# Kernel tuning notes

Measured on AMD Instinct MI355X. Metric: run time of the kernel, lower is better.

Reference implementation:

```python
import jax, jax.numpy as jnp
import numpy as np

N, E, F_IN, F_OUT, PERIODS = 40000, 640000, 64, 128, 12


def setup_inputs() -> dict:
    key = jax.random.key(0)
    ks = jax.random.split(key, 24)
    def w(k, shape):
        return jax.random.normal(k, shape, jnp.float32) * 0.05
    inp = {
        "X": jax.random.normal(ks[0], (N, F_IN, PERIODS), jnp.float32),
        "edge_index": jax.random.randint(ks[1], (2, E), 0, N),
        "edge_weight": jax.random.uniform(ks[2], (E,), jnp.float32),
        "attention": jax.random.uniform(ks[3], (PERIODS,), jnp.float32),
    }
    for idx, g in enumerate(["i", "f", "c", "o"]):
        inp[f"W_x{g}"] = w(ks[4 + 4 * idx], (F_IN, F_OUT))
        inp[f"b_x{g}"] = jnp.zeros((F_OUT,), jnp.float32)
        inp[f"W_h{g}"] = w(ks[5 + 4 * idx], (2 * F_OUT, F_OUT))
        inp[f"b_h{g}"] = jnp.zeros((F_OUT,), jnp.float32)
    return inp


def reference(X, edge_index, edge_weight, attention,
              W_xi, b_xi, W_hi, b_hi,
              W_xf, b_xf, W_hf, b_hf,
              W_xc, b_xc, W_hc, b_hc,
              W_xo, b_xo, W_ho, b_ho):
    n = X.shape[0]
    # GCN normalization with self-loops: D^-1/2 (A + I) D^-1/2
    loops = jnp.arange(n)
    rows = jnp.concatenate([edge_index[0], loops])  # sources
    cols = jnp.concatenate([edge_index[1], loops])  # targets
    wts = jnp.concatenate([edge_weight, jnp.ones((n,), X.dtype)])
    deg = jax.ops.segment_sum(wts, cols, num_segments=n)
    dinv = jnp.where(deg > 0, jax.lax.rsqrt(deg), 0.0)
    norm = dinv[rows] * wts * dinv[cols]  # [E+N]

    def gcn(x, W, b):
        xw = x @ W  # [N, F_OUT]
        agg = jax.ops.segment_sum(norm[:, None] * xw[rows], cols, num_segments=n)
        return agg + b

    probs = jax.nn.softmax(attention)
    H0 = jnp.zeros((n, W_hi.shape[1]), X.dtype)
    C0 = jnp.zeros_like(H0)
    Xp = jnp.moveaxis(X, 2, 0)  # [periods, N, F_IN]

    def step(carry, xs):
        H, C, Hacc = carry
        x_t, p = xs
        def gate(Wx, bx, Wh, bh):
            return jnp.concatenate([gcn(x_t, Wx, bx), H], axis=1) @ Wh + bh
        I = jax.nn.sigmoid(gate(W_xi, b_xi, W_hi, b_hi))
        F = jax.nn.sigmoid(gate(W_xf, b_xf, W_hf, b_hf))
        Ct = jnp.tanh(gate(W_xc, b_xc, W_hc, b_hc))
        O = jax.nn.sigmoid(gate(W_xo, b_xo, W_ho, b_ho))
        C_new = F * C + I * Ct
        H_new = O * jnp.tanh(C_new)
        return (H_new, C_new, Hacc + p * H_new), None

    (H, C, Hacc), _ = jax.lax.scan(step, (H0, C0, H0), (Xp, probs))
    return Hacc
```

## Files before the change

### kernel.cpp

```cpp
#include <hip/hip_runtime.h>

typedef __bf16 bf16_t;
typedef bf16_t bf16x4 __attribute__((ext_vector_type(4)));
typedef bf16_t bf16x8 __attribute__((ext_vector_type(8)));
typedef float floatx4 __attribute__((ext_vector_type(4)));

#define F_INq 64
#define F_OUTq 128
#define PERIODSq 12
#define XROW (F_INq * PERIODSq)

__global__ __launch_bounds__(256) void k_init(float* deg, int* counts, int N) {
  int i = blockIdx.x * 256 + threadIdx.x;
  if (i < N) { deg[i] = 1.0f; counts[i] = 0; }
}

__global__ __launch_bounds__(256) void k_accum(const int* __restrict__ ei, const float* __restrict__ ew,
                                               float* deg, int* counts, int E) {
  int e = blockIdx.x * 256 + threadIdx.x;
  if (e < E) {
    int c = ei[E + e];
    atomicAdd(&deg[c], ew[e]);
    atomicAdd(&counts[c], 1);
  }
}

__global__ __launch_bounds__(256) void k_dinv(float* deg, int N) {
  int i = blockIdx.x * 256 + threadIdx.x;
  if (i < N) { float d = deg[i]; deg[i] = d > 0.0f ? rsqrtf(d) : 0.0f; }
}

__global__ __launch_bounds__(1024) void k_scan(const int* __restrict__ counts, int* __restrict__ offs,
                                               int* __restrict__ cursor, int N) {
  __shared__ int sd[1024];
  int t = threadIdx.x;
  int CH = (N + 1023) >> 10;
  int base = t * CH;
  int sum = 0;
  for (int i = 0; i < CH; ++i) { int idx = base + i; if (idx < N) sum += counts[idx]; }
  sd[t] = sum;
  __syncthreads();
  for (int off = 1; off < 1024; off <<= 1) {
    int v = (t >= off) ? sd[t - off] : 0;
    __syncthreads();
    sd[t] += v;
    __syncthreads();
  }
  int run = sd[t] - sum;
  for (int i = 0; i < CH; ++i) {
    int idx = base + i;
    if (idx < N) { offs[idx] = run; cursor[idx] = run; run += counts[idx]; }
  }
  if (t == 1023) offs[N] = sd[1023];
}

__global__ __launch_bounds__(256) void k_scatter(const int* __restrict__ ei, const float* __restrict__ ew,
                                                 const float* __restrict__ dinv, int* cursor,
                                                 int* __restrict__ csr_src, float* __restrict__ csr_nrm, int E) {
  int e = blockIdx.x * 256 + threadIdx.x;
  if (e < E) {
    int r = ei[e], c = ei[E + e];
    int p = atomicAdd(&cursor[c], 1);
    csr_src[p] = r;
    csr_nrm[p] = dinv[r] * ew[e] * dinv[c];
  }
}

__global__ __launch_bounds__(256) void k_prew(
    const float* __restrict__ Wxi, const float* __restrict__ Whi,
    const float* __restrict__ Wxf, const float* __restrict__ Whf,
    const float* __restrict__ Wxc, const float* __restrict__ Whc,
    const float* __restrict__ Wxo, const float* __restrict__ Who,
    const float* __restrict__ bxi, const float* __restrict__ bhi,
    const float* __restrict__ bxf, const float* __restrict__ bhf,
    const float* __restrict__ bxc, const float* __restrict__ bhc,
    const float* __restrict__ bxo, const float* __restrict__ bho,
    const float* __restrict__ att,
    bf16_t* __restrict__ WbT, float* __restrict__ bcomb, float* __restrict__ probs) {
  const int WT = 512 * 192;
  int gid = blockIdx.x * 256 + threadIdx.x;
  if (gid < WT) {
    int col = gid / 192, k = gid % 192;
    int g = col >> 7, j = col & 127;
    const float* Wx = g == 0 ? Wxi : g == 1 ? Wxf : g == 2 ? Wxc : Wxo;
    const float* Wh = g == 0 ? Whi : g == 1 ? Whf : g == 2 ? Whc : Who;
    float s;
    if (k < 64) {
      s = 0.0f;
      for (int kk = 0; kk < 128; ++kk) s += Wx[k * 128 + kk] * Wh[kk * 128 + j];
    } else {
      s = Wh[(k + 64) * 128 + j];
    }
    WbT[(size_t)col * 192 + k] = (bf16_t)s;
  } else if (gid < WT + 512) {
    int cc = gid - WT;
    int g = cc >> 7, j = cc & 127;
    const float* bx = g == 0 ? bxi : g == 1 ? bxf : g == 2 ? bxc : bxo;
    const float* bh = g == 0 ? bhi : g == 1 ? bhf : g == 2 ? bhc : bho;
    const float* Wh = g == 0 ? Whi : g == 1 ? Whf : g == 2 ? Whc : Who;
    float s = bh[j];
    for (int kk = 0; kk < 128; ++kk) s += bx[kk] * Wh[kk * 128 + j];
    bcomb[cc] = s;
  } else if (gid == WT + 512) {
    float m = att[0];
    for (int i = 1; i < PERIODSq; ++i) m = fmaxf(m, att[i]);
    float e[PERIODSq], s = 0.0f;
    for (int i = 0; i < PERIODSq; ++i) { e[i] = __expf(att[i] - m); s += e[i]; }
    for (int i = 0; i < PERIODSq; ++i) probs[i] = e[i] / s;
  }
}

__global__ __launch_bounds__(192) void k_xpose(const float* __restrict__ X, bf16_t* __restrict__ Xb) {
  __shared__ float lds[XROW];
  const int n = blockIdx.x, tid = threadIdx.x;
  const float4* Xr = (const float4*)(X + (size_t)n * XROW);
  float4 v = Xr[tid];
  lds[tid * 4 + 0] = v.x;
  lds[tid * 4 + 1] = v.y;
  lds[tid * 4 + 2] = v.z;
  lds[tid * 4 + 3] = v.w;
  __syncthreads();
  const int o = tid * 4;
  bf16x4 r;
#pragma unroll
  for (int k = 0; k < 4; ++k) {
    int oo = o + k;
    int tt = oo >> 6, f = oo & 63;
    r[k] = (bf16_t)lds[f * PERIODSq + tt];
  }
  *(bf16x4*)(Xb + (size_t)n * XROW + o) = r;
}

__global__ __launch_bounds__(256) void k_agg2(const bf16_t* __restrict__ Xb, const int* __restrict__ csr_src,
                                              const float* __restrict__ csr_nrm, const int* __restrict__ offs,
                                              const float* __restrict__ dinv, bf16_t* __restrict__ Xagg, int N) {
  const int node = blockIdx.x * 4 + (threadIdx.x >> 6);
  const int lane = threadIdx.x & 63;
  const int s0 = offs[node], s1 = offs[node + 1];
  floatx4 a0 = {0.f, 0.f, 0.f, 0.f}, a1 = a0, a2 = a0;
  int e = s0;
  for (; e + 8 <= s1; e += 8) {
    bf16x4 v[8][3];
    float nn[8];
#pragma unroll
    for (int u = 0; u < 8; ++u) {
      int s = csr_src[e + u];
      nn[u] = csr_nrm[e + u];
      const bf16x4* xp = (const bf16x4*)(Xb + (size_t)s * XROW) + lane;
      v[u][0] = xp[0]; v[u][1] = xp[64]; v[u][2] = xp[128];
    }
#pragma unroll
    for (int u = 0; u < 8; ++u) {
#pragma unroll
      for (int k = 0; k < 4; ++k) {
        a0[k] += nn[u] * (float)v[u][0][k];
        a1[k] += nn[u] * (float)v[u][1][k];
        a2[k] += nn[u] * (float)v[u][2][k];
      }
    }
  }
  for (; e < s1; ++e) {
    int s = csr_src[e];
    float nr = csr_nrm[e];
    const bf16x4* xp = (const bf16x4*)(Xb + (size_t)s * XROW) + lane;
    bf16x4 v0 = xp[0], v1 = xp[64], v2 = xp[128];
#pragma unroll
    for (int k = 0; k < 4; ++k) {
      a0[k] += nr * (float)v0[k];
      a1[k] += nr * (float)v1[k];
      a2[k] += nr * (float)v2[k];
    }
  }
  float dc = dinv[node];
  float self = dc * dc;
  const bf16x4* xc = (const bf16x4*)(Xb + (size_t)node * XROW) + lane;
  {
    bf16x4 v0 = xc[0], v1 = xc[64], v2 = xc[128];
#pragma unroll
    for (int k = 0; k < 4; ++k) {
      a0[k] += self * (float)v0[k];
      a1[k] += self * (float)v1[k];
      a2[k] += self * (float)v2[k];
    }
  }
  const int f4 = lane & 15, tq = lane >> 4;
  floatx4 accs[3] = {a0, a1, a2};
#pragma unroll
  for (int j = 0; j < 3; ++j) {
    int tt = tq + 4 * j;
    bf16x4 r;
#pragma unroll
    for (int k = 0; k < 4; ++k) r[k] = (bf16_t)accs[j][k];
    *(bf16x4*)(Xagg + ((size_t)tt * N + node) * 64 + f4 * 4) = r;
  }
}

__global__ __launch_bounds__(256) void k_agg(const float* __restrict__ X, const int* __restrict__ csr_src,
                                             const float* __restrict__ csr_nrm, const int* __restrict__ offs,
                                             const float* __restrict__ dinv, bf16_t* __restrict__ Xagg, int N) {
  int c = blockIdx.x;
  int tid = threadIdx.x;
  int s0 = offs[c], s1 = offs[c + 1];
  const int i0 = tid, i1 = tid + 256, i2 = tid + 512;
  float a0 = 0.f, a1 = 0.f, a2 = 0.f;
  for (int e = s0; e < s1; ++e) {
    int s = csr_src[e];
    float nr = csr_nrm[e];
    const float* xp = X + (size_t)s * XROW;
    a0 += nr * xp[i0]; a1 += nr * xp[i1]; a2 += nr * xp[i2];
  }
  float dc = dinv[c];
  float self = dc * dc;
  const float* xc = X + (size_t)c * XROW;
  a0 += self * xc[i0]; a1 += self * xc[i1]; a2 += self * xc[i2];
  __shared__ float lds[XROW];
  lds[i0] = a0; lds[i1] = a1; lds[i2] = a2;
  __syncthreads();
  for (int o = tid; o < XROW; o += 256) {
    int tt = o >> 6, f = o & 63;
    Xagg[(size_t)tt * N * 64 + (size_t)c * 64 + f] = (bf16_t)lds[f * PERIODSq + tt];
  }
}

#define HS_P 130
__global__ __launch_bounds__(512, 2) void k_gate_all(const bf16_t* __restrict__ Xagg,
                                                     const bf16_t* __restrict__ WbT,
                                                     const float* __restrict__ bcomb,
                                                     const float* __restrict__ probs,
                                                     float* __restrict__ out, int N) {
  __shared__ bf16_t Hs[32][HS_P];
  __shared__ float biasS[512];
  __shared__ float probsS[16];
  const int tid = threadIdx.x;
  const int lane = tid & 63, w = tid >> 6;
  const int q = lane >> 4, c0 = lane & 15;
  const int n0 = blockIdx.x * 32;

  biasS[tid] = bcomb[tid];
  if (tid < PERIODSq) probsS[tid] = probs[tid];
  for (int i = tid; i < 32 * HS_P / 2; i += 512) ((unsigned int*)&Hs[0][0])[i] = 0u;

  bf16x8 Wf[4][6];
#pragma unroll
  for (int g = 0; g < 4; ++g) {
    const bf16_t* wp = WbT + (size_t)((g * 8 + w) * 16 + c0) * 192;
#pragma unroll
    for (int ks = 0; ks < 6; ++ks) Wf[g][ks] = *(const bf16x8*)(wp + ks * 32 + q * 8);
  }
  floatx4 Cst[2], Ha[2];
#pragma unroll
  for (int rt = 0; rt < 2; ++rt) {
    Cst[rt] = (floatx4){0.f, 0.f, 0.f, 0.f};
    Ha[rt] = (floatx4){0.f, 0.f, 0.f, 0.f};
  }
  __syncthreads();

  const float NL2E = -1.44269504f;
  const float T2L2E = 2.88539008f;
  const bf16_t* Xrow0 = Xagg + (size_t)(n0 + c0) * 64 + q * 8;
  const bf16_t* Xrow1 = Xagg + (size_t)(n0 + 16 + c0) * 64 + q * 8;

  for (int t = 0; t < PERIODSq; ++t) {
    const size_t toff = (size_t)t * N * 64;
    bf16x8 X00 = *(const bf16x8*)(Xrow0 + toff);
    bf16x8 X01 = *(const bf16x8*)(Xrow0 + toff + 32);
    bf16x8 X10 = *(const bf16x8*)(Xrow1 + toff);
    bf16x8 X11 = *(const bf16x8*)(Xrow1 + toff + 32);

    floatx4 acc[2][4];
#pragma unroll
    for (int rt = 0; rt < 2; ++rt)
#pragma unroll
      for (int g = 0; g < 4; ++g) acc[rt][g] = (floatx4){0.f, 0.f, 0.f, 0.f};

#pragma unroll
    for (int ks = 0; ks < 4; ++ks) {
      bf16x8 B0 = *(const bf16x8*)&Hs[c0][ks * 32 + q * 8];
      bf16x8 B1 = *(const bf16x8*)&Hs[16 + c0][ks * 32 + q * 8];
#pragma unroll
      for (int g = 0; g < 4; ++g) {
        acc[0][g] = __builtin_amdgcn_mfma_f32_16x16x32_bf16(Wf[g][ks + 2], B0, acc[0][g], 0, 0, 0);
        acc[1][g] = __builtin_amdgcn_mfma_f32_16x16x32_bf16(Wf[g][ks + 2], B1, acc[1][g], 0, 0, 0);
      }
    }
#pragma unroll
    for (int g = 0; g < 4; ++g) {
      acc[0][g] = __builtin_amdgcn_mfma_f32_16x16x32_bf16(Wf[g][0], X00, acc[0][g], 0, 0, 0);
      acc[1][g] = __builtin_amdgcn_mfma_f32_16x16x32_bf16(Wf[g][0], X10, acc[1][g], 0, 0, 0);
      acc[0][g] = __builtin_amdgcn_mfma_f32_16x16x32_bf16(Wf[g][1], X01, acc[0][g], 0, 0, 0);
      acc[1][g] = __builtin_amdgcn_mfma_f32_16x16x32_bf16(Wf[g][1], X11, acc[1][g], 0, 0, 0);
    }
    __syncthreads();

    const float pt = probsS[t];
#pragma unroll
    for (int rt = 0; rt < 2; ++rt) {
      bf16x4 hv;
#pragma unroll
      for (int r = 0; r < 4; ++r) {
        float pI = acc[rt][0][r] + biasS[0 + w * 16 + q * 4 + r];
        float pF = acc[rt][1][r] + biasS[128 + w * 16 + q * 4 + r];
        float pC = acc[rt][2][r] + biasS[256 + w * 16 + q * 4 + r];
        float pO = acc[rt][3][r] + biasS[384 + w * 16 + q * 4 + r];
        float I = __builtin_amdgcn_rcpf(1.0f + __builtin_amdgcn_exp2f(pI * NL2E));
        float F = __builtin_amdgcn_rcpf(1.0f + __builtin_amdgcn_exp2f(pF * NL2E));
        float Ct = fmaf(-2.0f, __builtin_amdgcn_rcpf(1.0f + __builtin_amdgcn_exp2f(pC * T2L2E)), 1.0f);
        float O = __builtin_amdgcn_rcpf(1.0f + __builtin_amdgcn_exp2f(pO * NL2E));
        float Cn = fmaf(F, Cst[rt][r], I * Ct);
        Cst[rt][r] = Cn;
        float tC = fmaf(-2.0f, __builtin_amdgcn_rcpf(1.0f + __builtin_amdgcn_exp2f(Cn * T2L2E)), 1.0f);
        float Hn = O * tC;
        Ha[rt][r] = fmaf(pt, Hn, Ha[rt][r]);
        hv[r] = (bf16_t)Hn;
      }
      *(bf16x4*)&Hs[rt * 16 + c0][w * 16 + q * 4] = hv;
    }
    __syncthreads();
  }
#pragma unroll
  for (int rt = 0; rt < 2; ++rt) {
    int row = n0 + rt * 16 + c0;
    *(floatx4*)(out + (size_t)row * 128 + w * 16 + q * 4) = Ha[rt];
  }
}

extern "C" void kernel_launch(void* const* d_in, const int* in_sizes, int n_in,
                              void* d_out, int out_size, void* d_ws, size_t ws_size,
                              hipStream_t stream) {
  const float* X = (const float*)d_in[0];
  const int* ei = (const int*)d_in[1];
  const float* ew = (const float*)d_in[2];
  const float* att = (const float*)d_in[3];
  const float* Wxi = (const float*)d_in[4];
  const float* bxi = (const float*)d_in[5];
  const float* Whi = (const float*)d_in[6];
  const float* bhi = (const float*)d_in[7];
  const float* Wxf = (const float*)d_in[8];
  const float* bxf = (const float*)d_in[9];
  const float* Whf = (const float*)d_in[10];
  const float* bhf = (const float*)d_in[11];
  const float* Wxc = (const float*)d_in[12];
  const float* bxc = (const float*)d_in[13];
  const float* Whc = (const float*)d_in[14];
  const float* bhc = (const float*)d_in[15];
  const float* Wxo = (const float*)d_in[16];
  const float* bxo = (const float*)d_in[17];
  const float* Who = (const float*)d_in[18];
  const float* bho = (const float*)d_in[19];
  float* out = (float*)d_out;

  const int N = in_sizes[0] / XROW;
  const int E = in_sizes[2];

  char* base = (char*)d_ws;
  size_t off = 0;
  auto carve = [&](size_t bytes) {
    char* r = base + off;
    off += (bytes + 255) & ~(size_t)255;
    return (void*)r;
  };
  float* deg = (float*)carve((size_t)N * 4);
  int* counts = (int*)carve((size_t)N * 4);
  int* offs = (int*)carve((size_t)(N + 1) * 4);
  int* cursor = (int*)carve((size_t)(N + 1) * 4);
  int* csr_src = (int*)carve((size_t)E * 4);
  float* csr_nrm = (float*)carve((size_t)E * 4);
  bf16_t* WbT = (bf16_t*)carve((size_t)512 * 192 * 2);
  float* bcomb = (float*)carve(512 * 4);
  float* probs = (float*)carve(64);
  bf16_t* Xagg = (bf16_t*)carve((size_t)PERIODSq * N * 64 * 2);
  bf16_t* Xb = (bf16_t*)carve((size_t)N * XROW * 2);
  const bool use_bf16 = (off <= ws_size);

  k_init<<<(N + 255) / 256, 256, 0, stream>>>(deg, counts, N);
  k_accum<<<(E + 255) / 256, 256, 0, stream>>>(ei, ew, deg, counts, E);
  k_dinv<<<(N + 255) / 256, 256, 0, stream>>>(deg, N);
  k_scan<<<1, 1024, 0, stream>>>(counts, offs, cursor, N);
  k_scatter<<<(E + 255) / 256, 256, 0, stream>>>(ei, ew, deg, cursor, csr_src, csr_nrm, E);
  k_prew<<<(512 * 192 + 512 + 1 + 255) / 256, 256, 0, stream>>>(
      Wxi, Whi, Wxf, Whf, Wxc, Whc, Wxo, Who,
      bxi, bhi, bxf, bhf, bxc, bhc, bxo, bho, att, WbT, bcomb, probs);

  if (use_bf16) {
    k_xpose<<<N, 192, 0, stream>>>(X, Xb);
    k_agg2<<<N / 4, 256, 0, stream>>>(Xb, csr_src, csr_nrm, offs, deg, Xagg, N);
  } else {
    k_agg<<<N, 256, 0, stream>>>(X, csr_src, csr_nrm, offs, deg, Xagg, N);
  }

  k_gate_all<<<N / 32, 512, 0, stream>>>(Xagg, WbT, bcomb, probs, out, N);
}
```

Measured before the change: 747.8 us.

## Pipeline LSTM gate kernel with double-buffered swizzled H and parallel CSR scan

The single-block 1024-thread prefix scan is replaced by a three-kernel multi-block scan that uses wave shuffles. In the gate kernel, the hidden state moves to double-buffered, XOR-swizzled shared memory, so only one barrier per period is needed and bank conflicts drop. The X-projection MFMAs and the global loads for the next period are issued during the current period's activation math. Biases are folded into the accumulator initialisation, and probs are read directly. Holding two accumulator sets raises register pressure, which could hurt occupancy at two blocks of 512 threads.

```diff
diff --git a/kernel.cpp b/kernel.cpp
--- a/kernel.cpp
+++ b/kernel.cpp
@@ -28,6 +28,70 @@
 __global__ __launch_bounds__(256) void k_dinv(float* deg, int N) {
   int i = blockIdx.x * 256 + threadIdx.x;
   if (i < N) { float d = deg[i]; deg[i] = d > 0.0f ? rsqrtf(d) : 0.0f; }
+}
+
+__global__ __launch_bounds__(256) void k_scanA(const int* __restrict__ counts, int* __restrict__ bsum, int N) {
+  __shared__ int ws[4];
+  int b = blockIdx.x, t = threadIdx.x;
+  int base = b * 1024 + t * 4;
+  int s = 0;
+  if (base + 3 < N) {
+    int4 c = *(const int4*)(counts + base);
+    s = c.x + c.y + c.z + c.w;
+  } else {
+    for (int k = 0; k < 4; ++k) if (base + k < N) s += counts[base + k];
+  }
+  for (int off = 1; off < 64; off <<= 1) s += __shfl_xor(s, off);
+  int lane = t & 63, w = t >> 6;
+  if (lane == 0) ws[w] = s;
+  __syncthreads();
+  if (t == 0) bsum[b] = ws[0] + ws[1] + ws[2] + ws[3];
+}
+
+__global__ __launch_bounds__(64) void k_scanB(const int* __restrict__ bsum, int* __restrict__ bbase, int nb) {
+  int t = threadIdx.x;
+  int v = t < nb ? bsum[t] : 0;
+  int inc = v;
+  for (int off = 1; off < 64; off <<= 1) {
+    int u = __shfl_up(inc, off);
+    if (t >= off) inc += u;
+  }
+  if (t < nb) bbase[t] = inc - v;
+  if (t == nb - 1) bbase[nb] = inc;
+}
+
+__global__ __launch_bounds__(256) void k_scanC(const int* __restrict__ counts, const int* __restrict__ bbase,
+                                               int* __restrict__ offs, int* __restrict__ cursor, int N, int nb) {
+  __shared__ int ws[4];
+  int b = blockIdx.x, t = threadIdx.x;
+  int base = b * 1024 + t * 4;
+  int c0_ = 0, c1_ = 0, c2_ = 0, c3_ = 0;
+  if (base + 3 < N) {
+    int4 c = *(const int4*)(counts + base);
+    c0_ = c.x; c1_ = c.y; c2_ = c.z; c3_ = c.w;
+  } else {
+    if (base < N) c0_ = counts[base];
+    if (base + 1 < N) c1_ = counts[base + 1];
+    if (base + 2 < N) c2_ = counts[base + 2];
+    if (base + 3 < N) c3_ = counts[base + 3];
+  }
+  int tot = c0_ + c1_ + c2_ + c3_;
+  int lane = t & 63, w = t >> 6;
+  int inc = tot;
+  for (int off = 1; off < 64; off <<= 1) {
+    int u = __shfl_up(inc, off);
+    if (lane >= off) inc += u;
+  }
+  if (lane == 63) ws[w] = inc;
+  __syncthreads();
+  int wb = bbase[b];
+  for (int i = 0; i < w; ++i) wb += ws[i];
+  int e = wb + inc - tot;
+  if (base < N)     { offs[base] = e;                 cursor[base] = e; }
+  if (base + 1 < N) { int o = e + c0_;                offs[base + 1] = o; cursor[base + 1] = o; }
+  if (base + 2 < N) { int o = e + c0_ + c1_;          offs[base + 2] = o; cursor[base + 2] = o; }
+  if (base + 3 < N) { int o = e + c0_ + c1_ + c2_;    offs[base + 3] = o; cursor[base + 3] = o; }
+  if (b == 0 && t == 0) offs[N] = bbase[nb];
 }
 
 __global__ __launch_bounds__(1024) void k_scan(const int* __restrict__ counts, int* __restrict__ offs,
@@ -222,23 +286,17 @@
   }
 }
 
-#define HS_P 130
 __global__ __launch_bounds__(512, 2) void k_gate_all(const bf16_t* __restrict__ Xagg,
                                                      const bf16_t* __restrict__ WbT,
                                                      const float* __restrict__ bcomb,
                                                      const float* __restrict__ probs,
                                                      float* __restrict__ out, int N) {
-  __shared__ bf16_t Hs[32][HS_P];
-  __shared__ float biasS[512];
-  __shared__ float probsS[16];
+  __shared__ __align__(16) char Hs[2][32 * 256];
   const int tid = threadIdx.x;
   const int lane = tid & 63, w = tid >> 6;
   const int q = lane >> 4, c0 = lane & 15;
   const int n0 = blockIdx.x * 32;
-
-  biasS[tid] = bcomb[tid];
-  if (tid < PERIODSq) probsS[tid] = probs[tid];
-  for (int i = tid; i < 32 * HS_P / 2; i += 512) ((unsigned int*)&Hs[0][0])[i] = 0u;
+  const int swz = c0 & 7;
 
   bf16x8 Wf[4][6];
 #pragma unroll
@@ -247,76 +305,96 @@
 #pragma unroll
     for (int ks = 0; ks < 6; ++ks) Wf[g][ks] = *(const bf16x8*)(wp + ks * 32 + q * 8);
   }
+  floatx4 bv[4];
+#pragma unroll
+  for (int g = 0; g < 4; ++g) bv[g] = *(const floatx4*)(bcomb + g * 128 + w * 16 + q * 4);
+
   floatx4 Cst[2], Ha[2];
 #pragma unroll
   for (int rt = 0; rt < 2; ++rt) {
     Cst[rt] = (floatx4){0.f, 0.f, 0.f, 0.f};
     Ha[rt] = (floatx4){0.f, 0.f, 0.f, 0.f};
   }
-  __syncthreads();
+
+  const bf16_t* Xrow0 = Xagg + (size_t)(n0 + c0) * 64 + q * 8;
+  const bf16_t* Xrow1 = Xagg + (size_t)(n0 + 16 + c0) * 64 + q * 8;
+
+  bf16x8 Xf0 = *(const bf16x8*)(Xrow0);
+  bf16x8 Xf1 = *(const bf16x8*)(Xrow0 + 32);
+  bf16x8 Xf2 = *(const bf16x8*)(Xrow1);
+  bf16x8 Xf3 = *(const bf16x8*)(Xrow1 + 32);
+
+  floatx4 accA[2][4], accB[2][4];
+#pragma unroll
+  for (int g = 0; g < 4; ++g) { accA[0][g] = bv[g]; accA[1][g] = bv[g]; }
+#pragma unroll
+  for (int g = 0; g < 4; ++g) {
+    accA[0][g] = __builtin_amdgcn_mfma_f32_16x16x32_bf16(Wf[g][0], Xf0, accA[0][g], 0, 0, 0);
+    accA[0][g] = __builtin_amdgcn_mfma_f32_16x16x32_bf16(Wf[g][1], Xf1, accA[0][g], 0, 0, 0);
+    accA[1][g] = __builtin_amdgcn_mfma_f32_16x16x32_bf16(Wf[g][0], Xf2, accA[1][g], 0, 0, 0);
+    accA[1][g] = __builtin_amdgcn_mfma_f32_16x16x32_bf16(Wf[g][1], Xf3, accA[1][g], 0, 0, 0);
+  }
 
   const float NL2E = -1.44269504f;
   const float T2L2E = 2.88539008f;
-  const bf16_t* Xrow0 = Xagg + (size_t)(n0 + c0) * 64 + q * 8;
-  const bf16_t* Xrow1 = Xagg + (size_t)(n0 + 16 + c0) * 64 + q * 8;
-
-  for (int t = 0; t < PERIODSq; ++t) {
-    const size_t toff = (size_t)t * N * 64;
-    bf16x8 X00 = *(const bf16x8*)(Xrow0 + toff);
-    bf16x8 X01 = *(const bf16x8*)(Xrow0 + toff + 32);
-    bf16x8 X10 = *(const bf16x8*)(Xrow1 + toff);
-    bf16x8 X11 = *(const bf16x8*)(Xrow1 + toff + 32);
-
-    floatx4 acc[2][4];
-#pragma unroll
-    for (int rt = 0; rt < 2; ++rt)
-#pragma unroll
-      for (int g = 0; g < 4; ++g) acc[rt][g] = (floatx4){0.f, 0.f, 0.f, 0.f};
-
-#pragma unroll
-    for (int ks = 0; ks < 4; ++ks) {
-      bf16x8 B0 = *(const bf16x8*)&Hs[c0][ks * 32 + q * 8];
-      bf16x8 B1 = *(const bf16x8*)&Hs[16 + c0][ks * 32 + q * 8];
-#pragma unroll
-      for (int g = 0; g < 4; ++g) {
-        acc[0][g] = __builtin_amdgcn_mfma_f32_16x16x32_bf16(Wf[g][ks + 2], B0, acc[0][g], 0, 0, 0);
-        acc[1][g] = __builtin_amdgcn_mfma_f32_16x16x32_bf16(Wf[g][ks + 2], B1, acc[1][g], 0, 0, 0);
-      }
-    }
-#pragma unroll
-    for (int g = 0; g < 4; ++g) {
-      acc[0][g] = __builtin_amdgcn_mfma_f32_16x16x32_bf16(Wf[g][0], X00, acc[0][g], 0, 0, 0);
-      acc[1][g] = __builtin_amdgcn_mfma_f32_16x16x32_bf16(Wf[g][0], X10, acc[1][g], 0, 0, 0);
-      acc[0][g] = __builtin_amdgcn_mfma_f32_16x16x32_bf16(Wf[g][1], X01, acc[0][g], 0, 0, 0);
-      acc[1][g] = __builtin_amdgcn_mfma_f32_16x16x32_bf16(Wf[g][1], X11, acc[1][g], 0, 0, 0);
-    }
-    __syncthreads();
-
-    const float pt = probsS[t];
-#pragma unroll
-    for (int rt = 0; rt < 2; ++rt) {
-      bf16x4 hv;
-#pragma unroll
-      for (int r = 0; r < 4; ++r) {
-        float pI = acc[rt][0][r] + biasS[0 + w * 16 + q * 4 + r];
-        float pF = acc[rt][1][r] + biasS[128 + w * 16 + q * 4 + r];
-        float pC = acc[rt][2][r] + biasS[256 + w * 16 + q * 4 + r];
-        float pO = acc[rt][3][r] + biasS[384 + w * 16 + q * 4 + r];
-        float I = __builtin_amdgcn_rcpf(1.0f + __builtin_amdgcn_exp2f(pI * NL2E));
-        float F = __builtin_amdgcn_rcpf(1.0f + __builtin_amdgcn_exp2f(pF * NL2E));
-        float Ct = fmaf(-2.0f, __builtin_amdgcn_rcpf(1.0f + __builtin_amdgcn_exp2f(pC * T2L2E)), 1.0f);
-        float O = __builtin_amdgcn_rcpf(1.0f + __builtin_amdgcn_exp2f(pO * NL2E));
-        float Cn = fmaf(F, Cst[rt][r], I * Ct);
-        Cst[rt][r] = Cn;
-        float tC = fmaf(-2.0f, __builtin_amdgcn_rcpf(1.0f + __builtin_amdgcn_exp2f(Cn * T2L2E)), 1.0f);
-        float Hn = O * tC;
-        Ha[rt][r] = fmaf(pt, Hn, Ha[rt][r]);
-        hv[r] = (bf16_t)Hn;
-      }
-      *(bf16x4*)&Hs[rt * 16 + c0][w * 16 + q * 4] = hv;
-    }
-    __syncthreads();
-  }
+
+#define PERIOD(T, AC, AN, RB, WB, DO_H, DO_NEXT)                                                      \
+  do {                                                                                                \
+    if (DO_NEXT) {                                                                                    \
+      const size_t toff_ = (size_t)((T) + 1) * N * 64;                                                \
+      Xf0 = *(const bf16x8*)(Xrow0 + toff_);                                                          \
+      Xf1 = *(const bf16x8*)(Xrow0 + toff_ + 32);                                                     \
+      Xf2 = *(const bf16x8*)(Xrow1 + toff_);                                                          \
+      Xf3 = *(const bf16x8*)(Xrow1 + toff_ + 32);                                                     \
+    }                                                                                                 \
+    if (DO_H) {                                                                                       \
+      _Pragma("unroll") for (int ks = 0; ks < 4; ++ks) {                                              \
+        bf16x8 B0 = *(const bf16x8*)(&Hs[RB][(c0) * 256 + (((4 * ks + q) ^ swz) << 4)]);              \
+        bf16x8 B1 = *(const bf16x8*)(&Hs[RB][(16 + c0) * 256 + (((4 * ks + q) ^ swz) << 4)]);         \
+        _Pragma("unroll") for (int g = 0; g < 4; ++g) {                                               \
+          AC[0][g] = __builtin_amdgcn_mfma_f32_16x16x32_bf16(Wf[g][ks + 2], B0, AC[0][g], 0, 0, 0);   \
+          AC[1][g] = __builtin_amdgcn_mfma_f32_16x16x32_bf16(Wf[g][ks + 2], B1, AC[1][g], 0, 0, 0);   \
+        }                                                                                             \
+      }                                                                                               \
+    }                                                                                                 \
+    const float pt_ = probs[T];                                                                       \
+    _Pragma("unroll") for (int rt = 0; rt < 2; ++rt) {                                                \
+      bf16x4 hv_;                                                                                     \
+      _Pragma("unroll") for (int r = 0; r < 4; ++r) {                                                 \
+        float pI = AC[rt][0][r], pF = AC[rt][1][r], pC = AC[rt][2][r], pO = AC[rt][3][r];             \
+        float I_ = __builtin_amdgcn_rcpf(1.0f + __builtin_amdgcn_exp2f(pI * NL2E));                   \
+        float F_ = __builtin_amdgcn_rcpf(1.0f + __builtin_amdgcn_exp2f(pF * NL2E));                   \
+        float Ct_ = fmaf(-2.0f, __builtin_amdgcn_rcpf(1.0f + __builtin_amdgcn_exp2f(pC * T2L2E)), 1.0f); \
+        float O_ = __builtin_amdgcn_rcpf(1.0f + __builtin_amdgcn_exp2f(pO * NL2E));                   \
+        float Cn_ = fmaf(F_, Cst[rt][r], I_ * Ct_);                                                   \
+        Cst[rt][r] = Cn_;                                                                             \
+        float tC_ = fmaf(-2.0f, __builtin_amdgcn_rcpf(1.0f + __builtin_amdgcn_exp2f(Cn_ * T2L2E)), 1.0f); \
+        float Hn_ = O_ * tC_;                                                                         \
+        Ha[rt][r] = fmaf(pt_, Hn_, Ha[rt][r]);                                                        \
+        hv_[r] = (bf16_t)Hn_;                                                                         \
+      }                                                                                               \
+      *(bf16x4*)(&Hs[WB][(rt * 16 + c0) * 256 + (((2 * w + (q >> 1)) ^ swz) << 4) + ((q & 1) * 8)]) = hv_; \
+    }                                                                                                 \
+    if (DO_NEXT) {                                                                                    \
+      _Pragma("unroll") for (int g = 0; g < 4; ++g) { AN[0][g] = bv[g]; AN[1][g] = bv[g]; }           \
+      _Pragma("unroll") for (int g = 0; g < 4; ++g) {                                                 \
+        AN[0][g] = __builtin_amdgcn_mfma_f32_16x16x32_bf16(Wf[g][0], Xf0, AN[0][g], 0, 0, 0);         \
+        AN[0][g] = __builtin_amdgcn_mfma_f32_16x16x32_bf16(Wf[g][1], Xf1, AN[0][g], 0, 0, 0);         \
+        AN[1][g] = __builtin_amdgcn_mfma_f32_16x16x32_bf16(Wf[g][0], Xf2, AN[1][g], 0, 0, 0);         \
+        AN[1][g] = __builtin_amdgcn_mfma_f32_16x16x32_bf16(Wf[g][1], Xf3, AN[1][g], 0, 0, 0);         \
+      }                                                                                               \
+    }                                                                                                 \
+    __syncthreads();                                                                                  \
+  } while (0)
+
+  PERIOD(0, accA, accB, 1, 0, 0, 1);
+  for (int tt = 1; tt <= 9; tt += 2) {
+    PERIOD(tt, accB, accA, 0, 1, 1, 1);
+    PERIOD(tt + 1, accA, accB, 1, 0, 1, 1);
+  }
+  PERIOD(11, accB, accA, 0, 1, 1, 0);
+#undef PERIOD
+
 #pragma unroll
   for (int rt = 0; rt < 2; ++rt) {
     int row = n0 + rt * 16 + c0;
@@ -368,6 +446,8 @@
   bf16_t* WbT = (bf16_t*)carve((size_t)512 * 192 * 2);
   float* bcomb = (float*)carve(512 * 4);
   float* probs = (float*)carve(64);
+  int* bsum = (int*)carve(64 * 4);
+  int* bbase = (int*)carve(68 * 4);
   bf16_t* Xagg = (bf16_t*)carve((size_t)PERIODSq * N * 64 * 2);
   bf16_t* Xb = (bf16_t*)carve((size_t)N * XROW * 2);
   const bool use_bf16 = (off <= ws_size);
@@ -375,7 +455,14 @@
   k_init<<<(N + 255) / 256, 256, 0, stream>>>(deg, counts, N);
   k_accum<<<(E + 255) / 256, 256, 0, stream>>>(ei, ew, deg, counts, E);
   k_dinv<<<(N + 255) / 256, 256, 0, stream>>>(deg, N);
-  k_scan<<<1, 1024, 0, stream>>>(counts, offs, cursor, N);
+  const int nb = (N + 1023) >> 10;
+  if (nb <= 64) {
+    k_scanA<<<nb, 256, 0, stream>>>(counts, bsum, N);
+    k_scanB<<<1, 64, 0, stream>>>(bsum, bbase, nb);
+    k_scanC<<<nb, 256, 0, stream>>>(counts, bbase, offs, cursor, N, nb);
+  } else {
+    k_scan<<<1, 1024, 0, stream>>>(counts, offs, cursor, N);
+  }
   k_scatter<<<(E + 255) / 256, 256, 0, stream>>>(ei, ew, deg, cursor, csr_src, csr_nrm, E);
   k_prew<<<(512 * 192 + 512 + 1 + 255) / 256, 256, 0, stream>>>(
       Wxi, Whi, Wxf, Whf, Wxc, Whc, Wxo, Who,
```

Result: faster. 604.5 us (-19.2%).
